# Optimization experiments

Measured on AMD Instinct MI355X. Metric: run time of the kernel, lower is better.

The kernel has to match this reference:

```python
import jax, jax.numpy as jnp
import numpy as np

B, N, K, C, D_IN, D_OUT = 64, 207, 32, 8, 64, 64


def setup_inputs() -> dict:
    key = jax.random.key(0)
    k1, k2, k3 = jax.random.split(key, 3)
    clustered_index_topk = jax.random.randint(k1, (B, N, K), 0, C)
    weightedDinput_topk = jax.random.normal(k2, (B, N, K, D_IN), dtype=jnp.float32)
    W = jax.random.normal(k3, (C, D_OUT, D_IN), dtype=jnp.float32) * 0.05
    return {"clustered_index_topk": clustered_index_topk,
            "weightedDinput_topk": weightedDinput_topk,
            "W": W}


def reference(clustered_index_topk, weightedDinput_topk, W):
    # one-hot over classes: [B, N, K, C]
    onehot = (clustered_index_topk[..., None] == jnp.arange(C)).astype(weightedDinput_topk.dtype)
    # per-class masked sum over top-k neighbors: [B, N, C, D_IN]
    sums = jnp.einsum('bnkc,bnkd->bncd', onehot, weightedDinput_topk)
    # per-class counts, clamped to >= 1 (matches torch.clamp(class_count, 1))
    counts = jnp.maximum(onehot.sum(axis=2), 1.0)  # [B, N, C]
    mean = sums / counts[..., None]
    # per-class Linear (weight [out, in], no bias) + Tanh -> [B, N, C, D_OUT]
    out = jnp.tanh(jnp.einsum('bncd,cod->bnco', mean, W))
    return out
```

## Files before the change

kernel.cpp:

```cpp
#include <hip/hip_runtime.h>
#include <cstddef>

#define BB 64
#define NN 207
#define KK 32
#define CC 8
#define DIN 64
#define DOUT 64
#define TILE 16
#define NT ((NN + TILE - 1) / TILE)
#define MPAD 68

__device__ __forceinline__ float fast_tanh(float v) {
    float e = __expf(2.0f * v);
    return 1.0f - 2.0f * __builtin_amdgcn_rcpf(e + 1.0f);
}

__global__ __launch_bounds__(256) void transpose_W_kernel(
    const float* __restrict__ W, float* __restrict__ Wt)
{
    __shared__ float t[DIN * (DOUT + 1)];
    const int c   = blockIdx.x;
    const int tid = threadIdx.x;
    const float* __restrict__ Wc  = W  + (size_t)c * DOUT * DIN;
    float* __restrict__       Wtc = Wt + (size_t)c * DIN * DOUT;
    #pragma unroll
    for (int r = 0; r < 16; ++r) {
        const int i = r * 256 + tid;
        const int o = i >> 6, d = i & 63;
        t[d * (DOUT + 1) + o] = Wc[i];
    }
    __syncthreads();
    #pragma unroll
    for (int r = 0; r < 16; ++r) {
        const int i = r * 256 + tid;
        const int d = i >> 6, o = i & 63;
        Wtc[i] = t[d * (DOUT + 1) + o];
    }
}

template<bool USE_WT>
__global__ __launch_bounds__(256, 4) void ordered_gcn_kernel(
    const int* __restrict__ idx,
    const float* __restrict__ x,
    const float* __restrict__ W,
    const float* __restrict__ Wt,
    float* __restrict__ out)
{
    __shared__ int   idx_s[TILE * KK];
    __shared__ float inv_s[TILE * CC];
    __shared__ float mean_s[TILE * CC * MPAD];

    const int tid = threadIdx.x;
    const int b  = blockIdx.y;
    const int n0 = blockIdx.x * TILE;

    #pragma unroll
    for (int r = 0; r < 2; ++r) {
        const int i = r * 256 + tid;
        const int p = i >> 5, k = i & 31;
        int n = n0 + p; if (n > NN - 1) n = NN - 1;
        idx_s[i] = idx[((size_t)(b * NN + n)) * KK + k];
    }
    __syncthreads();

    if (tid < TILE * CC) {
        const int pp = tid >> 3, c = tid & 7;
        int cnt = 0;
        #pragma unroll
        for (int k = 0; k < KK; ++k) cnt += (idx_s[pp * KK + k] == c) ? 1 : 0;
        inv_s[tid] = 1.0f / (float)(cnt > 1 ? cnt : 1);
    }

    const int p  = tid >> 4;
    const int d4 = (tid & 15) * 4;
    {
        int n = n0 + p; if (n > NN - 1) n = NN - 1;
        const float* __restrict__ xp = x + ((size_t)(b * NN + n)) * KK * DIN + d4;

        float4 acc[CC];
        #pragma unroll
        for (int c = 0; c < CC; ++c) acc[c] = make_float4(0.f, 0.f, 0.f, 0.f);

        #pragma unroll 1
        for (int g = 0; g < 4; ++g) {
            float4 v[8];
            #pragma unroll
            for (int j = 0; j < 8; ++j)
                v[j] = *(const float4*)(xp + (size_t)(g * 8 + j) * DIN);
            #pragma unroll
            for (int j = 0; j < 8; ++j) {
                const int ca = idx_s[p * KK + g * 8 + j];
                #pragma unroll
                for (int cc_ = 0; cc_ < CC; ++cc_) {
                    const float mf = (ca == cc_) ? 1.0f : 0.0f;
                    acc[cc_].x = fmaf(mf, v[j].x, acc[cc_].x);
                    acc[cc_].y = fmaf(mf, v[j].y, acc[cc_].y);
                    acc[cc_].z = fmaf(mf, v[j].z, acc[cc_].z);
                    acc[cc_].w = fmaf(mf, v[j].w, acc[cc_].w);
                }
            }
        }
        __syncthreads();

        #pragma unroll
        for (int cc_ = 0; cc_ < CC; ++cc_) {
            const float s = inv_s[p * CC + cc_];
            float4 m;
            m.x = acc[cc_].x * s; m.y = acc[cc_].y * s;
            m.z = acc[cc_].z * s; m.w = acc[cc_].w * s;
            *(float4*)(&mean_s[(p * CC + cc_) * MPAD + d4]) = m;
        }
    }
    __syncthreads();

    {
        const int ph = tid >> 7;
        const int c  = (tid >> 4) & 7;
        const int o0 = (tid & 15) * 4;

        float4 acc2[8];
        #pragma unroll
        for (int pp = 0; pp < 8; ++pp) acc2[pp] = make_float4(0.f, 0.f, 0.f, 0.f);

        if (USE_WT) {
            const float* __restrict__ Wtc = Wt + (size_t)c * DIN * DOUT + o0;
            #pragma unroll 1
            for (int dc = 0; dc < 16; ++dc) {
                const float4 w0 = *(const float4*)(Wtc + (size_t)(dc * 4 + 0) * DOUT);
                const float4 w1 = *(const float4*)(Wtc + (size_t)(dc * 4 + 1) * DOUT);
                const float4 w2 = *(const float4*)(Wtc + (size_t)(dc * 4 + 2) * DOUT);
                const float4 w3 = *(const float4*)(Wtc + (size_t)(dc * 4 + 3) * DOUT);
                #pragma unroll
                for (int pp = 0; pp < 8; ++pp) {
                    const int pq = ph * 8 + pp;
                    const float4 m = *(const float4*)(&mean_s[(pq * CC + c) * MPAD + dc * 4]);
                    acc2[pp].x = fmaf(m.x, w0.x, acc2[pp].x);
                    acc2[pp].y = fmaf(m.x, w0.y, acc2[pp].y);
                    acc2[pp].z = fmaf(m.x, w0.z, acc2[pp].z);
                    acc2[pp].w = fmaf(m.x, w0.w, acc2[pp].w);
                    acc2[pp].x = fmaf(m.y, w1.x, acc2[pp].x);
                    acc2[pp].y = fmaf(m.y, w1.y, acc2[pp].y);
                    acc2[pp].z = fmaf(m.y, w1.z, acc2[pp].z);
                    acc2[pp].w = fmaf(m.y, w1.w, acc2[pp].w);
                    acc2[pp].x = fmaf(m.z, w2.x, acc2[pp].x);
                    acc2[pp].y = fmaf(m.z, w2.y, acc2[pp].y);
                    acc2[pp].z = fmaf(m.z, w2.z, acc2[pp].z);
                    acc2[pp].w = fmaf(m.z, w2.w, acc2[pp].w);
                    acc2[pp].x = fmaf(m.w, w3.x, acc2[pp].x);
                    acc2[pp].y = fmaf(m.w, w3.y, acc2[pp].y);
                    acc2[pp].z = fmaf(m.w, w3.z, acc2[pp].z);
                    acc2[pp].w = fmaf(m.w, w3.w, acc2[pp].w);
                }
            }
        } else {
            const float* __restrict__ Wc = W + (size_t)c * DOUT * DIN;
            #pragma unroll 1
            for (int dc = 0; dc < 16; ++dc) {
                float4 w[4];
                #pragma unroll
                for (int j = 0; j < 4; ++j)
                    w[j] = *(const float4*)(Wc + (size_t)(o0 + j) * DIN + dc * 4);
                #pragma unroll
                for (int pp = 0; pp < 8; ++pp) {
                    const int pq = ph * 8 + pp;
                    const float4 m = *(const float4*)(&mean_s[(pq * CC + c) * MPAD + dc * 4]);
                    float* a = (float*)&acc2[pp];
                    #pragma unroll
                    for (int j = 0; j < 4; ++j) {
                        a[j] = fmaf(m.x, w[j].x, a[j]);
                        a[j] = fmaf(m.y, w[j].y, a[j]);
                        a[j] = fmaf(m.z, w[j].z, a[j]);
                        a[j] = fmaf(m.w, w[j].w, a[j]);
                    }
                }
            }
        }

        #pragma unroll
        for (int pp = 0; pp < 8; ++pp) {
            const int pq = ph * 8 + pp;
            const int nn = n0 + pq;
            if (nn < NN) {
                float4 r;
                r.x = fast_tanh(acc2[pp].x);
                r.y = fast_tanh(acc2[pp].y);
                r.z = fast_tanh(acc2[pp].z);
                r.w = fast_tanh(acc2[pp].w);
                *(float4*)(out + (((size_t)(b * NN + nn)) * CC + c) * DOUT + o0) = r;
            }
        }
    }
}

extern "C" void kernel_launch(void* const* d_in, const int* in_sizes, int n_in,
                              void* d_out, int out_size, void* d_ws, size_t ws_size,
                              hipStream_t stream) {
    const int*   idx = (const int*)d_in[0];
    const float* x   = (const float*)d_in[1];
    const float* W   = (const float*)d_in[2];
    float* out = (float*)d_out;
    float* Wt  = (float*)d_ws;

    dim3 grid(NT, BB);
    dim3 block(256);
    const size_t wt_bytes = (size_t)CC * DIN * DOUT * sizeof(float);
    if (ws_size >= wt_bytes) {
        transpose_W_kernel<<<dim3(CC), block, 0, stream>>>(W, Wt);
        ordered_gcn_kernel<true><<<grid, block, 0, stream>>>(idx, x, W, Wt, out);
    } else {
        ordered_gcn_kernel<false><<<grid, block, 0, stream>>>(idx, x, W, Wt, out);
    }
}
```

Measured before the change: 184.0 us.

## Split fused kernel into mean pass and per-class GEMM+tanh pass via output buffer

The fused kernel is split in two. The first kernel computes class means over a flat (B*N) index space, which drops the padded-tile clamping, and writes them into the output buffer. The second kernel loads each class's W transposed into shared memory and runs the GEMM plus tanh in place, overwriting the means. This removes the separate transpose launch and the mean shared-memory staging, but adds a global round trip of the means tensor and one extra launch. The in-place overwrite is safe only because each thread reads its full row before writing it.

```diff
diff --git a/kernel.cpp b/kernel.cpp
--- a/kernel.cpp
+++ b/kernel.cpp
@@ -7,64 +7,26 @@
 #define CC 8
 #define DIN 64
 #define DOUT 64
-#define TILE 16
-#define NT ((NN + TILE - 1) / TILE)
-#define MPAD 68
+#define MM (BB * NN)
 
-__device__ __forceinline__ float fast_tanh(float v) {
-    float e = __expf(2.0f * v);
-    return 1.0f - 2.0f * __builtin_amdgcn_rcpf(e + 1.0f);
-}
-
-__global__ __launch_bounds__(256) void transpose_W_kernel(
-    const float* __restrict__ W, float* __restrict__ Wt)
-{
-    __shared__ float t[DIN * (DOUT + 1)];
-    const int c   = blockIdx.x;
-    const int tid = threadIdx.x;
-    const float* __restrict__ Wc  = W  + (size_t)c * DOUT * DIN;
-    float* __restrict__       Wtc = Wt + (size_t)c * DIN * DOUT;
-    #pragma unroll
-    for (int r = 0; r < 16; ++r) {
-        const int i = r * 256 + tid;
-        const int o = i >> 6, d = i & 63;
-        t[d * (DOUT + 1) + o] = Wc[i];
-    }
-    __syncthreads();
-    #pragma unroll
-    for (int r = 0; r < 16; ++r) {
-        const int i = r * 256 + tid;
-        const int d = i >> 6, o = i & 63;
-        Wtc[i] = t[d * (DOUT + 1) + o];
-    }
-}
-
-template<bool USE_WT>
-__global__ __launch_bounds__(256, 4) void ordered_gcn_kernel(
+#define MA 16
+__global__ __launch_bounds__(256) void mean_kernel(
     const int* __restrict__ idx,
     const float* __restrict__ x,
-    const float* __restrict__ W,
-    const float* __restrict__ Wt,
-    float* __restrict__ out)
+    float* __restrict__ mean)
 {
-    __shared__ int   idx_s[TILE * KK];
-    __shared__ float inv_s[TILE * CC];
-    __shared__ float mean_s[TILE * CC * MPAD];
+    __shared__ int   idx_s[MA * KK];
+    __shared__ float inv_s[MA * CC];
 
     const int tid = threadIdx.x;
-    const int b  = blockIdx.y;
-    const int n0 = blockIdx.x * TILE;
+    const int m0  = blockIdx.x * MA;
 
     #pragma unroll
-    for (int r = 0; r < 2; ++r) {
-        const int i = r * 256 + tid;
-        const int p = i >> 5, k = i & 31;
-        int n = n0 + p; if (n > NN - 1) n = NN - 1;
-        idx_s[i] = idx[((size_t)(b * NN + n)) * KK + k];
-    }
+    for (int r = 0; r < 2; ++r)
+        idx_s[r * 256 + tid] = idx[(size_t)m0 * KK + r * 256 + tid];
     __syncthreads();
 
-    if (tid < TILE * CC) {
+    if (tid < MA * CC) {
         const int pp = tid >> 3, c = tid & 7;
         int cnt = 0;
         #pragma unroll
@@ -74,122 +36,119 @@
 
     const int p  = tid >> 4;
     const int d4 = (tid & 15) * 4;
-    {
-        int n = n0 + p; if (n > NN - 1) n = NN - 1;
-        const float* __restrict__ xp = x + ((size_t)(b * NN + n)) * KK * DIN + d4;
+    const float* __restrict__ xp = x + ((size_t)(m0 + p)) * KK * DIN + d4;
 
-        float4 acc[CC];
+    float4 acc[CC];
+    #pragma unroll
+    for (int c = 0; c < CC; ++c) acc[c] = make_float4(0.f, 0.f, 0.f, 0.f);
+
+    #pragma unroll 1
+    for (int g = 0; g < 4; ++g) {
+        float4 v[8];
         #pragma unroll
-        for (int c = 0; c < CC; ++c) acc[c] = make_float4(0.f, 0.f, 0.f, 0.f);
-
-        #pragma unroll 1
-        for (int g = 0; g < 4; ++g) {
-            float4 v[8];
+        for (int j = 0; j < 8; ++j)
+            v[j] = *(const float4*)(xp + (size_t)(g * 8 + j) * DIN);
+        #pragma unroll
+        for (int j = 0; j < 8; ++j) {
+            const int ca = idx_s[p * KK + g * 8 + j];
             #pragma unroll
-            for (int j = 0; j < 8; ++j)
-                v[j] = *(const float4*)(xp + (size_t)(g * 8 + j) * DIN);
-            #pragma unroll
-            for (int j = 0; j < 8; ++j) {
-                const int ca = idx_s[p * KK + g * 8 + j];
-                #pragma unroll
-                for (int cc_ = 0; cc_ < CC; ++cc_) {
-                    const float mf = (ca == cc_) ? 1.0f : 0.0f;
-                    acc[cc_].x = fmaf(mf, v[j].x, acc[cc_].x);
-                    acc[cc_].y = fmaf(mf, v[j].y, acc[cc_].y);
-                    acc[cc_].z = fmaf(mf, v[j].z, acc[cc_].z);
-                    acc[cc_].w = fmaf(mf, v[j].w, acc[cc_].w);
-                }
+            for (int cc_ = 0; cc_ < CC; ++cc_) {
+                const float mf = (ca == cc_) ? 1.0f : 0.0f;
+                acc[cc_].x = fmaf(mf, v[j].x, acc[cc_].x);
+                acc[cc_].y = fmaf(mf, v[j].y, acc[cc_].y);
+                acc[cc_].z = fmaf(mf, v[j].z, acc[cc_].z);
+                acc[cc_].w = fmaf(mf, v[j].w, acc[cc_].w);
             }
-        }
-        __syncthreads();
-
-        #pragma unroll
-        for (int cc_ = 0; cc_ < CC; ++cc_) {
-            const float s = inv_s[p * CC + cc_];
-            float4 m;
-            m.x = acc[cc_].x * s; m.y = acc[cc_].y * s;
-            m.z = acc[cc_].z * s; m.w = acc[cc_].w * s;
-            *(float4*)(&mean_s[(p * CC + cc_) * MPAD + d4]) = m;
         }
     }
     __syncthreads();
 
-    {
-        const int ph = tid >> 7;
-        const int c  = (tid >> 4) & 7;
-        const int o0 = (tid & 15) * 4;
+    #pragma unroll
+    for (int cc_ = 0; cc_ < CC; ++cc_) {
+        const float s = inv_s[p * CC + cc_];
+        float4 m;
+        m.x = acc[cc_].x * s; m.y = acc[cc_].y * s;
+        m.z = acc[cc_].z * s; m.w = acc[cc_].w * s;
+        *(float4*)(mean + (((size_t)(m0 + p)) * CC + cc_) * DIN + d4) = m;
+    }
+}
 
-        float4 acc2[8];
+__device__ __forceinline__ float fast_tanh(float v) {
+    float e = __expf(2.0f * v);
+    return 1.0f - 2.0f * __builtin_amdgcn_rcpf(e + 1.0f);
+}
+
+#define PB 6
+#define MBLK (16 * PB)
+#define WPAD 68
+__global__ __launch_bounds__(256) void gemm_tanh_kernel(
+    const float* __restrict__ W,
+    float* io)
+{
+    __shared__ float wt[DIN * WPAD];
+
+    const int tid = threadIdx.x;
+    const int c   = blockIdx.y;
+    const int m0  = blockIdx.x * MBLK;
+
+    const float* __restrict__ Wc = W + (size_t)c * DOUT * DIN;
+    #pragma unroll
+    for (int r = 0; r < 16; ++r) {
+        const int i = r * 256 + tid;
+        const int o = i >> 6, d = i & 63;
+        wt[d * WPAD + o] = Wc[i];
+    }
+    __syncthreads();
+
+    const int g  = tid >> 4;
+    const int o4 = (tid & 15) * 4;
+
+    float4 acc[PB];
+    #pragma unroll
+    for (int r = 0; r < PB; ++r) acc[r] = make_float4(0.f, 0.f, 0.f, 0.f);
+
+    #pragma unroll 1
+    for (int dc = 0; dc < 16; ++dc) {
+        const float4 w0 = *(const float4*)(&wt[(dc * 4 + 0) * WPAD + o4]);
+        const float4 w1 = *(const float4*)(&wt[(dc * 4 + 1) * WPAD + o4]);
+        const float4 w2 = *(const float4*)(&wt[(dc * 4 + 2) * WPAD + o4]);
+        const float4 w3 = *(const float4*)(&wt[(dc * 4 + 3) * WPAD + o4]);
+        float4 mv[PB];
         #pragma unroll
-        for (int pp = 0; pp < 8; ++pp) acc2[pp] = make_float4(0.f, 0.f, 0.f, 0.f);
+        for (int r = 0; r < PB; ++r) {
+            const int m = m0 + g + 16 * r;
+            mv[r] = *(const float4*)(io + ((size_t)m * CC + c) * DIN + dc * 4);
+        }
+        #pragma unroll
+        for (int r = 0; r < PB; ++r) {
+            acc[r].x = fmaf(mv[r].x, w0.x, acc[r].x);
+            acc[r].y = fmaf(mv[r].x, w0.y, acc[r].y);
+            acc[r].z = fmaf(mv[r].x, w0.z, acc[r].z);
+            acc[r].w = fmaf(mv[r].x, w0.w, acc[r].w);
+            acc[r].x = fmaf(mv[r].y, w1.x, acc[r].x);
+            acc[r].y = fmaf(mv[r].y, w1.y, acc[r].y);
+            acc[r].z = fmaf(mv[r].y, w1.z, acc[r].z);
+            acc[r].w = fmaf(mv[r].y, w1.w, acc[r].w);
+            acc[r].x = fmaf(mv[r].z, w2.x, acc[r].x);
+            acc[r].y = fmaf(mv[r].z, w2.y, acc[r].y);
+            acc[r].z = fmaf(mv[r].z, w2.z, acc[r].z);
+            acc[r].w = fmaf(mv[r].z, w2.w, acc[r].w);
+            acc[r].x = fmaf(mv[r].w, w3.x, acc[r].x);
+            acc[r].y = fmaf(mv[r].w, w3.y, acc[r].y);
+            acc[r].z = fmaf(mv[r].w, w3.z, acc[r].z);
+            acc[r].w = fmaf(mv[r].w, w3.w, acc[r].w);
+        }
+    }
 
-        if (USE_WT) {
-            const float* __restrict__ Wtc = Wt + (size_t)c * DIN * DOUT + o0;
-            #pragma unroll 1
-            for (int dc = 0; dc < 16; ++dc) {
-                const float4 w0 = *(const float4*)(Wtc + (size_t)(dc * 4 + 0) * DOUT);
-                const float4 w1 = *(const float4*)(Wtc + (size_t)(dc * 4 + 1) * DOUT);
-                const float4 w2 = *(const float4*)(Wtc + (size_t)(dc * 4 + 2) * DOUT);
-                const float4 w3 = *(const float4*)(Wtc + (size_t)(dc * 4 + 3) * DOUT);
-                #pragma unroll
-                for (int pp = 0; pp < 8; ++pp) {
-                    const int pq = ph * 8 + pp;
-                    const float4 m = *(const float4*)(&mean_s[(pq * CC + c) * MPAD + dc * 4]);
-                    acc2[pp].x = fmaf(m.x, w0.x, acc2[pp].x);
-                    acc2[pp].y = fmaf(m.x, w0.y, acc2[pp].y);
-                    acc2[pp].z = fmaf(m.x, w0.z, acc2[pp].z);
-                    acc2[pp].w = fmaf(m.x, w0.w, acc2[pp].w);
-                    acc2[pp].x = fmaf(m.y, w1.x, acc2[pp].x);
-                    acc2[pp].y = fmaf(m.y, w1.y, acc2[pp].y);
-                    acc2[pp].z = fmaf(m.y, w1.z, acc2[pp].z);
-                    acc2[pp].w = fmaf(m.y, w1.w, acc2[pp].w);
-                    acc2[pp].x = fmaf(m.z, w2.x, acc2[pp].x);
-                    acc2[pp].y = fmaf(m.z, w2.y, acc2[pp].y);
-                    acc2[pp].z = fmaf(m.z, w2.z, acc2[pp].z);
-                    acc2[pp].w = fmaf(m.z, w2.w, acc2[pp].w);
-                    acc2[pp].x = fmaf(m.w, w3.x, acc2[pp].x);
-                    acc2[pp].y = fmaf(m.w, w3.y, acc2[pp].y);
-                    acc2[pp].z = fmaf(m.w, w3.z, acc2[pp].z);
-                    acc2[pp].w = fmaf(m.w, w3.w, acc2[pp].w);
-                }
-            }
-        } else {
-            const float* __restrict__ Wc = W + (size_t)c * DOUT * DIN;
-            #pragma unroll 1
-            for (int dc = 0; dc < 16; ++dc) {
-                float4 w[4];
-                #pragma unroll
-                for (int j = 0; j < 4; ++j)
-                    w[j] = *(const float4*)(Wc + (size_t)(o0 + j) * DIN + dc * 4);
-                #pragma unroll
-                for (int pp = 0; pp < 8; ++pp) {
-                    const int pq = ph * 8 + pp;
-                    const float4 m = *(const float4*)(&mean_s[(pq * CC + c) * MPAD + dc * 4]);
-                    float* a = (float*)&acc2[pp];
-                    #pragma unroll
-                    for (int j = 0; j < 4; ++j) {
-                        a[j] = fmaf(m.x, w[j].x, a[j]);
-                        a[j] = fmaf(m.y, w[j].y, a[j]);
-                        a[j] = fmaf(m.z, w[j].z, a[j]);
-                        a[j] = fmaf(m.w, w[j].w, a[j]);
-                    }
-                }
-            }
-        }
-
-        #pragma unroll
-        for (int pp = 0; pp < 8; ++pp) {
-            const int pq = ph * 8 + pp;
-            const int nn = n0 + pq;
-            if (nn < NN) {
-                float4 r;
-                r.x = fast_tanh(acc2[pp].x);
-                r.y = fast_tanh(acc2[pp].y);
-                r.z = fast_tanh(acc2[pp].z);
-                r.w = fast_tanh(acc2[pp].w);
-                *(float4*)(out + (((size_t)(b * NN + nn)) * CC + c) * DOUT + o0) = r;
-            }
-        }
+    #pragma unroll
+    for (int r = 0; r < PB; ++r) {
+        const int m = m0 + g + 16 * r;
+        float4 o;
+        o.x = fast_tanh(acc[r].x);
+        o.y = fast_tanh(acc[r].y);
+        o.z = fast_tanh(acc[r].z);
+        o.w = fast_tanh(acc[r].w);
+        *(float4*)(io + ((size_t)m * CC + c) * DIN + o4) = o;
     }
 }
 
@@ -200,15 +159,9 @@
     const float* x   = (const float*)d_in[1];
     const float* W   = (const float*)d_in[2];
     float* out = (float*)d_out;
-    float* Wt  = (float*)d_ws;
 
-    dim3 grid(NT, BB);
-    dim3 block(256);
-    const size_t wt_bytes = (size_t)CC * DIN * DOUT * sizeof(float);
-    if (ws_size >= wt_bytes) {
-        transpose_W_kernel<<<dim3(CC), block, 0, stream>>>(W, Wt);
-        ordered_gcn_kernel<true><<<grid, block, 0, stream>>>(idx, x, W, Wt, out);
-    } else {
-        ordered_gcn_kernel<false><<<grid, block, 0, stream>>>(idx, x, W, Wt, out);
-    }
+    (void)d_ws; (void)ws_size;
+
+    mean_kernel<<<dim3(MM / MA), dim3(256), 0, stream>>>(idx, x, out);
+    gemm_tanh_kernel<<<dim3(MM / MBLK, CC), dim3(256), 0, stream>>>(W, out);
 }
```

Measured after the change: 198.7 us. +8.0%, slower.

## Flatten B*N into single-wave blocks of four points with in-register counts

Applied to the files above, without the earlier changes.

Each block is now a single 64-lane wave that handles 4 flattened (b,n) rows, launched as a 1D grid of 3312 blocks. This replaces the 16-row tiles over a 2D grid, which wasted work on clamped tail rows. Class counts are now accumulated in registers during the masked sum, which removes the separate count pass and one barrier. The linear stage has each thread loop over the 8 classes for its own row. W rows are therefore reloaded per row rather than reused across 8 rows, which raises global/L2 traffic for W in exchange for more parallelism and less shared-memory pressure.

```diff
diff --git a/kernel.cpp b/kernel.cpp
--- a/kernel.cpp
+++ b/kernel.cpp
@@ -7,8 +7,10 @@
 #define CC 8
 #define DIN 64
 #define DOUT 64
-#define TILE 16
-#define NT ((NN + TILE - 1) / TILE)
+#define MM (BB * NN)
+#define PW 4
+#define NBLK (MM / PW)
+#define IPAD 33
 #define MPAD 68
 
 __device__ __forceinline__ float fast_tanh(float v) {
@@ -40,156 +42,116 @@
 }
 
 template<bool USE_WT>
-__global__ __launch_bounds__(256, 4) void ordered_gcn_kernel(
+__global__ __launch_bounds__(64, 4) void ordered_gcn_kernel(
     const int* __restrict__ idx,
     const float* __restrict__ x,
     const float* __restrict__ W,
     const float* __restrict__ Wt,
     float* __restrict__ out)
 {
-    __shared__ int   idx_s[TILE * KK];
-    __shared__ float inv_s[TILE * CC];
-    __shared__ float mean_s[TILE * CC * MPAD];
+    __shared__ int   idx_s[PW * IPAD];
+    __shared__ float mean_s[CC * PW * MPAD];
 
-    const int tid = threadIdx.x;
-    const int b  = blockIdx.y;
-    const int n0 = blockIdx.x * TILE;
+    const int lane = threadIdx.x;
+    const int m0   = blockIdx.x * PW;
+    const int p    = lane >> 4;
+    const int q4   = (lane & 15) * 4;
 
-    #pragma unroll
-    for (int r = 0; r < 2; ++r) {
-        const int i = r * 256 + tid;
-        const int p = i >> 5, k = i & 31;
-        int n = n0 + p; if (n > NN - 1) n = NN - 1;
-        idx_s[i] = idx[((size_t)(b * NN + n)) * KK + k];
+    {
+        const int i0 = lane, i1 = lane + 64;
+        idx_s[(i0 >> 5) * IPAD + (i0 & 31)] = idx[(size_t)m0 * KK + i0];
+        idx_s[(i1 >> 5) * IPAD + (i1 & 31)] = idx[(size_t)m0 * KK + i1];
     }
     __syncthreads();
 
-    if (tid < TILE * CC) {
-        const int pp = tid >> 3, c = tid & 7;
-        int cnt = 0;
+    const float* __restrict__ xp = x + (size_t)(m0 + p) * KK * DIN + q4;
+    const int* idx_row = &idx_s[p * IPAD];
+
+    float4 acc[CC];
+    float  cntf[CC];
+    #pragma unroll
+    for (int c = 0; c < CC; ++c) { acc[c] = make_float4(0.f, 0.f, 0.f, 0.f); cntf[c] = 0.f; }
+
+    #pragma unroll 1
+    for (int g = 0; g < 4; ++g) {
+        float4 v[8];
         #pragma unroll
-        for (int k = 0; k < KK; ++k) cnt += (idx_s[pp * KK + k] == c) ? 1 : 0;
-        inv_s[tid] = 1.0f / (float)(cnt > 1 ? cnt : 1);
+        for (int j = 0; j < 8; ++j)
+            v[j] = *(const float4*)(xp + (size_t)(g * 8 + j) * DIN);
+        #pragma unroll
+        for (int j = 0; j < 8; ++j) {
+            const int ca = idx_row[g * 8 + j];
+            #pragma unroll
+            for (int cc_ = 0; cc_ < CC; ++cc_) {
+                const float mf = (ca == cc_) ? 1.0f : 0.0f;
+                cntf[cc_] += mf;
+                acc[cc_].x = fmaf(mf, v[j].x, acc[cc_].x);
+                acc[cc_].y = fmaf(mf, v[j].y, acc[cc_].y);
+                acc[cc_].z = fmaf(mf, v[j].z, acc[cc_].z);
+                acc[cc_].w = fmaf(mf, v[j].w, acc[cc_].w);
+            }
+        }
     }
 
-    const int p  = tid >> 4;
-    const int d4 = (tid & 15) * 4;
-    {
-        int n = n0 + p; if (n > NN - 1) n = NN - 1;
-        const float* __restrict__ xp = x + ((size_t)(b * NN + n)) * KK * DIN + d4;
-
-        float4 acc[CC];
-        #pragma unroll
-        for (int c = 0; c < CC; ++c) acc[c] = make_float4(0.f, 0.f, 0.f, 0.f);
-
-        #pragma unroll 1
-        for (int g = 0; g < 4; ++g) {
-            float4 v[8];
-            #pragma unroll
-            for (int j = 0; j < 8; ++j)
-                v[j] = *(const float4*)(xp + (size_t)(g * 8 + j) * DIN);
-            #pragma unroll
-            for (int j = 0; j < 8; ++j) {
-                const int ca = idx_s[p * KK + g * 8 + j];
-                #pragma unroll
-                for (int cc_ = 0; cc_ < CC; ++cc_) {
-                    const float mf = (ca == cc_) ? 1.0f : 0.0f;
-                    acc[cc_].x = fmaf(mf, v[j].x, acc[cc_].x);
-                    acc[cc_].y = fmaf(mf, v[j].y, acc[cc_].y);
-                    acc[cc_].z = fmaf(mf, v[j].z, acc[cc_].z);
-                    acc[cc_].w = fmaf(mf, v[j].w, acc[cc_].w);
-                }
-            }
-        }
-        __syncthreads();
-
-        #pragma unroll
-        for (int cc_ = 0; cc_ < CC; ++cc_) {
-            const float s = inv_s[p * CC + cc_];
-            float4 m;
-            m.x = acc[cc_].x * s; m.y = acc[cc_].y * s;
-            m.z = acc[cc_].z * s; m.w = acc[cc_].w * s;
-            *(float4*)(&mean_s[(p * CC + cc_) * MPAD + d4]) = m;
-        }
+    #pragma unroll
+    for (int c = 0; c < CC; ++c) {
+        const float s = 1.0f / fmaxf(cntf[c], 1.0f);
+        float4 m;
+        m.x = acc[c].x * s; m.y = acc[c].y * s;
+        m.z = acc[c].z * s; m.w = acc[c].w * s;
+        *(float4*)(&mean_s[(c * PW + p) * MPAD + q4]) = m;
     }
     __syncthreads();
 
-    {
-        const int ph = tid >> 7;
-        const int c  = (tid >> 4) & 7;
-        const int o0 = (tid & 15) * 4;
-
-        float4 acc2[8];
-        #pragma unroll
-        for (int pp = 0; pp < 8; ++pp) acc2[pp] = make_float4(0.f, 0.f, 0.f, 0.f);
+    #pragma unroll 1
+    for (int c = 0; c < CC; ++c) {
+        const float* mrow = &mean_s[(c * PW + p) * MPAD];
+        float4 a = make_float4(0.f, 0.f, 0.f, 0.f);
 
         if (USE_WT) {
-            const float* __restrict__ Wtc = Wt + (size_t)c * DIN * DOUT + o0;
-            #pragma unroll 1
+            const float* __restrict__ Wtc = Wt + (size_t)c * DIN * DOUT + q4;
+            #pragma unroll 2
             for (int dc = 0; dc < 16; ++dc) {
                 const float4 w0 = *(const float4*)(Wtc + (size_t)(dc * 4 + 0) * DOUT);
                 const float4 w1 = *(const float4*)(Wtc + (size_t)(dc * 4 + 1) * DOUT);
                 const float4 w2 = *(const float4*)(Wtc + (size_t)(dc * 4 + 2) * DOUT);
                 const float4 w3 = *(const float4*)(Wtc + (size_t)(dc * 4 + 3) * DOUT);
-                #pragma unroll
-                for (int pp = 0; pp < 8; ++pp) {
-                    const int pq = ph * 8 + pp;
-                    const float4 m = *(const float4*)(&mean_s[(pq * CC + c) * MPAD + dc * 4]);
-                    acc2[pp].x = fmaf(m.x, w0.x, acc2[pp].x);
-                    acc2[pp].y = fmaf(m.x, w0.y, acc2[pp].y);
-                    acc2[pp].z = fmaf(m.x, w0.z, acc2[pp].z);
-                    acc2[pp].w = fmaf(m.x, w0.w, acc2[pp].w);
-                    acc2[pp].x = fmaf(m.y, w1.x, acc2[pp].x);
-                    acc2[pp].y = fmaf(m.y, w1.y, acc2[pp].y);
-                    acc2[pp].z = fmaf(m.y, w1.z, acc2[pp].z);
-                    acc2[pp].w = fmaf(m.y, w1.w, acc2[pp].w);
-                    acc2[pp].x = fmaf(m.z, w2.x, acc2[pp].x);
-                    acc2[pp].y = fmaf(m.z, w2.y, acc2[pp].y);
-                    acc2[pp].z = fmaf(m.z, w2.z, acc2[pp].z);
-                    acc2[pp].w = fmaf(m.z, w2.w, acc2[pp].w);
-                    acc2[pp].x = fmaf(m.w, w3.x, acc2[pp].x);
-                    acc2[pp].y = fmaf(m.w, w3.y, acc2[pp].y);
-                    acc2[pp].z = fmaf(m.w, w3.z, acc2[pp].z);
-                    acc2[pp].w = fmaf(m.w, w3.w, acc2[pp].w);
-                }
+                const float4 m  = *(const float4*)(mrow + dc * 4);
+                a.x = fmaf(m.x, w0.x, a.x); a.y = fmaf(m.x, w0.y, a.y);
+                a.z = fmaf(m.x, w0.z, a.z); a.w = fmaf(m.x, w0.w, a.w);
+                a.x = fmaf(m.y, w1.x, a.x); a.y = fmaf(m.y, w1.y, a.y);
+                a.z = fmaf(m.y, w1.z, a.z); a.w = fmaf(m.y, w1.w, a.w);
+                a.x = fmaf(m.z, w2.x, a.x); a.y = fmaf(m.z, w2.y, a.y);
+                a.z = fmaf(m.z, w2.z, a.z); a.w = fmaf(m.z, w2.w, a.w);
+                a.x = fmaf(m.w, w3.x, a.x); a.y = fmaf(m.w, w3.y, a.y);
+                a.z = fmaf(m.w, w3.z, a.z); a.w = fmaf(m.w, w3.w, a.w);
             }
         } else {
             const float* __restrict__ Wc = W + (size_t)c * DOUT * DIN;
-            #pragma unroll 1
+            #pragma unroll 2
             for (int dc = 0; dc < 16; ++dc) {
                 float4 w[4];
                 #pragma unroll
                 for (int j = 0; j < 4; ++j)
-                    w[j] = *(const float4*)(Wc + (size_t)(o0 + j) * DIN + dc * 4);
+                    w[j] = *(const float4*)(Wc + (size_t)(q4 + j) * DIN + dc * 4);
+                const float4 m = *(const float4*)(mrow + dc * 4);
+                float* af = (float*)&a;
                 #pragma unroll
-                for (int pp = 0; pp < 8; ++pp) {
-                    const int pq = ph * 8 + pp;
-                    const float4 m = *(const float4*)(&mean_s[(pq * CC + c) * MPAD + dc * 4]);
-                    float* a = (float*)&acc2[pp];
-                    #pragma unroll
-                    for (int j = 0; j < 4; ++j) {
-                        a[j] = fmaf(m.x, w[j].x, a[j]);
-                        a[j] = fmaf(m.y, w[j].y, a[j]);
-                        a[j] = fmaf(m.z, w[j].z, a[j]);
-                        a[j] = fmaf(m.w, w[j].w, a[j]);
-                    }
+                for (int j = 0; j < 4; ++j) {
+                    af[j] = fmaf(m.x, w[j].x, af[j]);
+                    af[j] = fmaf(m.y, w[j].y, af[j]);
+                    af[j] = fmaf(m.z, w[j].z, af[j]);
+                    af[j] = fmaf(m.w, w[j].w, af[j]);
                 }
             }
         }
 
-        #pragma unroll
-        for (int pp = 0; pp < 8; ++pp) {
-            const int pq = ph * 8 + pp;
-            const int nn = n0 + pq;
-            if (nn < NN) {
-                float4 r;
-                r.x = fast_tanh(acc2[pp].x);
-                r.y = fast_tanh(acc2[pp].y);
-                r.z = fast_tanh(acc2[pp].z);
-                r.w = fast_tanh(acc2[pp].w);
-                *(float4*)(out + (((size_t)(b * NN + nn)) * CC + c) * DOUT + o0) = r;
-            }
-        }
+        float4 r;
+        r.x = fast_tanh(a.x);
+        r.y = fast_tanh(a.y);
+        r.z = fast_tanh(a.z);
+        r.w = fast_tanh(a.w);
+        *(float4*)(out + ((size_t)(m0 + p) * CC + c) * DOUT + q4) = r;
     }
 }
 
@@ -201,14 +163,11 @@
     const float* W   = (const float*)d_in[2];
     float* out = (float*)d_out;
     float* Wt  = (float*)d_ws;
-
-    dim3 grid(NT, BB);
-    dim3 block(256);
     const size_t wt_bytes = (size_t)CC * DIN * DOUT * sizeof(float);
     if (ws_size >= wt_bytes) {
-        transpose_W_kernel<<<dim3(CC), block, 0, stream>>>(W, Wt);
-        ordered_gcn_kernel<true><<<grid, block, 0, stream>>>(idx, x, W, Wt, out);
+        transpose_W_kernel<<<dim3(CC), dim3(256), 0, stream>>>(W, Wt);
+        ordered_gcn_kernel<true><<<dim3(NBLK), dim3(64), 0, stream>>>(idx, x, W, Wt, out);
     } else {
-        ordered_gcn_kernel<false><<<grid, block, 0, stream>>>(idx, x, W, Wt, out);
+        ordered_gcn_kernel<false><<<dim3(NBLK), dim3(64), 0, stream>>>(idx, x, W, Wt, out);
     }
 }
```

Result: slower. 223.7 us (+21.6%).

## Split top-k reduction across wave lanes with double-buffered loads and shuffle reduce

Applied to the files above, without the earlier changes.

The masked class-sum stage is reorganised so that each wavefront handles four points and splits the 32 neighbours across lane groups. Each lane group reads a contiguous 1KB chunk, giving fully coalesced loads. Partial sums are combined with cross-lane shuffles before being scaled and written to shared memory. Loads for the next point are issued while the current one is being accumulated, using two register buffers. This raises register pressure, so launch bounds drop to 2 blocks per SM, trading occupancy for more memory-level parallelism and better coalescing.

```diff
diff --git a/kernel.cpp b/kernel.cpp
--- a/kernel.cpp
+++ b/kernel.cpp
@@ -39,8 +39,54 @@
     }
 }
 
+__device__ __forceinline__ void pfw(float4 (&buf)[8], const float4* __restrict__ xp4,
+                                    int lane) {
+    #pragma unroll
+    for (int j = 0; j < 8; ++j)
+        buf[j] = xp4[j * 64 + lane];
+}
+__device__ __forceinline__ void cbw(float4 (&acc)[CC], const float4 (&buf)[8],
+                                    const int* idx_row, int kofs) {
+    #pragma unroll
+    for (int j = 0; j < 8; ++j) {
+        const int ca = idx_row[j * 4 + kofs];
+        #pragma unroll
+        for (int c = 0; c < CC; ++c) {
+            const float mf = (ca == c) ? 1.0f : 0.0f;
+            acc[c].x = fmaf(mf, buf[j].x, acc[c].x);
+            acc[c].y = fmaf(mf, buf[j].y, acc[c].y);
+            acc[c].z = fmaf(mf, buf[j].z, acc[c].z);
+            acc[c].w = fmaf(mf, buf[j].w, acc[c].w);
+        }
+    }
+}
+__device__ __forceinline__ void reduce_write(float4 (&acc)[CC], const float* inv_row,
+                                             float* mean_row_base, int lane, int d4) {
+    #pragma unroll
+    for (int c = 0; c < CC; ++c) {
+        acc[c].x += __shfl_xor(acc[c].x, 16);
+        acc[c].y += __shfl_xor(acc[c].y, 16);
+        acc[c].z += __shfl_xor(acc[c].z, 16);
+        acc[c].w += __shfl_xor(acc[c].w, 16);
+        acc[c].x += __shfl_xor(acc[c].x, 32);
+        acc[c].y += __shfl_xor(acc[c].y, 32);
+        acc[c].z += __shfl_xor(acc[c].z, 32);
+        acc[c].w += __shfl_xor(acc[c].w, 32);
+    }
+    if (lane < 16) {
+        #pragma unroll
+        for (int c = 0; c < CC; ++c) {
+            const float s = inv_row[c];
+            float4 m;
+            m.x = acc[c].x * s; m.y = acc[c].y * s;
+            m.z = acc[c].z * s; m.w = acc[c].w * s;
+            *(float4*)(mean_row_base + (size_t)c * MPAD + d4) = m;
+        }
+    }
+}
+
 template<bool USE_WT>
-__global__ __launch_bounds__(256, 4) void ordered_gcn_kernel(
+__global__ __launch_bounds__(256, 2) void ordered_gcn_kernel(
     const int* __restrict__ idx,
     const float* __restrict__ x,
     const float* __restrict__ W,
@@ -58,8 +104,8 @@
     #pragma unroll
     for (int r = 0; r < 2; ++r) {
         const int i = r * 256 + tid;
-        const int p = i >> 5, k = i & 31;
-        int n = n0 + p; if (n > NN - 1) n = NN - 1;
+        const int pq = i >> 5, k = i & 31;
+        int n = n0 + pq; if (n > NN - 1) n = NN - 1;
         idx_s[i] = idx[((size_t)(b * NN + n)) * KK + k];
     }
     __syncthreads();
@@ -71,46 +117,52 @@
         for (int k = 0; k < KK; ++k) cnt += (idx_s[pp * KK + k] == c) ? 1 : 0;
         inv_s[tid] = 1.0f / (float)(cnt > 1 ? cnt : 1);
     }
-
-    const int p  = tid >> 4;
-    const int d4 = (tid & 15) * 4;
+    __syncthreads();
+
     {
-        int n = n0 + p; if (n > NN - 1) n = NN - 1;
-        const float* __restrict__ xp = x + ((size_t)(b * NN + n)) * KK * DIN + d4;
+        const int wv   = tid >> 6;
+        const int lane = tid & 63;
+        const int kofs = lane >> 4;
+        const int d4   = (lane & 15) * 4;
+
+        const float4* xp[4];
+        #pragma unroll
+        for (int i = 0; i < 4; ++i) {
+            int n = n0 + wv * 4 + i; if (n > NN - 1) n = NN - 1;
+            xp[i] = (const float4*)(x + ((size_t)(b * NN + n)) * KK * DIN);
+        }
 
         float4 acc[CC];
-        #pragma unroll
-        for (int c = 0; c < CC; ++c) acc[c] = make_float4(0.f, 0.f, 0.f, 0.f);
-
-        #pragma unroll 1
-        for (int g = 0; g < 4; ++g) {
-            float4 v[8];
-            #pragma unroll
-            for (int j = 0; j < 8; ++j)
-                v[j] = *(const float4*)(xp + (size_t)(g * 8 + j) * DIN);
-            #pragma unroll
-            for (int j = 0; j < 8; ++j) {
-                const int ca = idx_s[p * KK + g * 8 + j];
-                #pragma unroll
-                for (int cc_ = 0; cc_ < CC; ++cc_) {
-                    const float mf = (ca == cc_) ? 1.0f : 0.0f;
-                    acc[cc_].x = fmaf(mf, v[j].x, acc[cc_].x);
-                    acc[cc_].y = fmaf(mf, v[j].y, acc[cc_].y);
-                    acc[cc_].z = fmaf(mf, v[j].z, acc[cc_].z);
-                    acc[cc_].w = fmaf(mf, v[j].w, acc[cc_].w);
-                }
-            }
-        }
-        __syncthreads();
-
-        #pragma unroll
-        for (int cc_ = 0; cc_ < CC; ++cc_) {
-            const float s = inv_s[p * CC + cc_];
-            float4 m;
-            m.x = acc[cc_].x * s; m.y = acc[cc_].y * s;
-            m.z = acc[cc_].z * s; m.w = acc[cc_].w * s;
-            *(float4*)(&mean_s[(p * CC + cc_) * MPAD + d4]) = m;
-        }
+        float4 va[8], vb[8];
+
+        pfw(va, xp[0], lane);
+        pfw(vb, xp[1], lane);
+
+        #pragma unroll
+        for (int c = 0; c < CC; ++c) acc[c] = make_float4(0.f, 0.f, 0.f, 0.f);
+        cbw(acc, va, &idx_s[(wv * 4 + 0) * KK], kofs);
+        pfw(va, xp[2], lane);
+        reduce_write(acc, &inv_s[(wv * 4 + 0) * CC],
+                     &mean_s[((wv * 4 + 0) * CC) * MPAD], lane, d4);
+
+        #pragma unroll
+        for (int c = 0; c < CC; ++c) acc[c] = make_float4(0.f, 0.f, 0.f, 0.f);
+        cbw(acc, vb, &idx_s[(wv * 4 + 1) * KK], kofs);
+        pfw(vb, xp[3], lane);
+        reduce_write(acc, &inv_s[(wv * 4 + 1) * CC],
+                     &mean_s[((wv * 4 + 1) * CC) * MPAD], lane, d4);
+
+        #pragma unroll
+        for (int c = 0; c < CC; ++c) acc[c] = make_float4(0.f, 0.f, 0.f, 0.f);
+        cbw(acc, va, &idx_s[(wv * 4 + 2) * KK], kofs);
+        reduce_write(acc, &inv_s[(wv * 4 + 2) * CC],
+                     &mean_s[((wv * 4 + 2) * CC) * MPAD], lane, d4);
+
+        #pragma unroll
+        for (int c = 0; c < CC; ++c) acc[c] = make_float4(0.f, 0.f, 0.f, 0.f);
+        cbw(acc, vb, &idx_s[(wv * 4 + 3) * KK], kofs);
+        reduce_write(acc, &inv_s[(wv * 4 + 3) * CC],
+                     &mean_s[((wv * 4 + 3) * CC) * MPAD], lane, d4);
     }
     __syncthreads();
 
@@ -201,7 +253,6 @@
     const float* W   = (const float*)d_in[2];
     float* out = (float*)d_out;
     float* Wt  = (float*)d_ws;
-
     dim3 grid(NT, BB);
     dim3 block(256);
     const size_t wt_bytes = (size_t)CC * DIN * DOUT * sizeof(float);
```

New measurement: 189.9 us. 3.2% more time.
